# Performance work log

Measured on AMD Instinct MI355X. Metric: run time of the kernel, lower is better.

The kernel has to match this reference:

```python
import jax, jax.numpy as jnp
import numpy as np

B, HQ, HK, S, D, HID, BS = 2, 32, 8, 8192, 128, 128, 16
NB = S // BS  # 512 pooled blocks


def rotate_half(x):
    h = x.shape[-1] // 2
    return jnp.concatenate([-x[..., h:], x[..., :h]], axis=-1)


def pool_cat(x):
    # avg + max pooling over block_size along the sequence dim, concat on feature dim
    b, h, s, d = x.shape
    xb = x.reshape(b, h, s // BS, BS, d)
    return jnp.concatenate([xb.mean(axis=3), xb.max(axis=3)], axis=-1)  # [b,h,NB,2d]


def setup_inputs() -> dict:
    key = jax.random.key(0)
    k0, k1, k2, k3 = jax.random.split(key, 4)
    q = jax.random.normal(k0, (B, HQ, S, D), jnp.float32)
    k = jax.random.normal(k1, (B, HK, S, D), jnp.float32)
    wq = jax.random.normal(k2, (HQ, 2 * D, HID), jnp.float32) / np.float32(np.sqrt(2 * D))
    wk = jax.random.normal(k3, (HK, 2 * D, HID), jnp.float32) / np.float32(np.sqrt(2 * D))
    # causal block mask
    mask = jnp.broadcast_to(jnp.tril(jnp.ones((NB, NB), bool))[None, None], (B, 1, NB, NB))
    # RoPE tables over pooled positions
    pos = jnp.arange(NB, dtype=jnp.float32)
    inv_freq = 1.0 / (10000.0 ** (jnp.arange(0, HID, 2, dtype=jnp.float32) / HID))
    freqs = pos[:, None] * inv_freq[None, :]              # [NB, HID/2]
    emb = jnp.concatenate([freqs, freqs], axis=-1)        # [NB, HID]
    cos = jnp.broadcast_to(jnp.cos(emb)[None], (B, NB, HID))
    sin = jnp.broadcast_to(jnp.sin(emb)[None], (B, NB, HID))
    return {"q": q, "k": k, "attention_mask": mask, "cos": cos, "sin": sin, "wq": wq, "wk": wk}


def reference(q, k, attention_mask, cos, sin, wq, wk):
    # pooled multi-head linear projections
    qh = jnp.einsum('bhnc,hcd->bhnd', pool_cat(q), wq)   # [B,HQ,NB,HID]
    kh = jnp.einsum('bhnc,hcd->bhnd', pool_cat(k), wk)   # [B,HK,NB,HID]
    # RoPE (unsqueeze_dim=1)
    c, s = cos[:, None], sin[:, None]
    qh = qh * c + rotate_half(qh) * s
    kh = kh * c + rotate_half(kh) * s
    # GQA: repeat kv heads
    kh = jnp.repeat(kh, HQ // HK, axis=1)                # [B,HQ,NB,HID]
    attn = jnp.einsum('bhqd,bhkd->bhqk', qh, kh) / jnp.sqrt(jnp.float32(HID))
    attn = jnp.where(attention_mask, attn, jnp.float32(-1e9))
    return jax.nn.softmax(attn, axis=-1)
```

## Files before the change

### kernel.cpp

```cpp
#include <hip/hip_runtime.h>

namespace {
constexpr int BB  = 2;
constexpr int HQ  = 32;
constexpr int HK  = 8;
constexpr int S   = 8192;
constexpr int D   = 128;
constexpr int HID = 128;
constexpr int BS  = 16;
constexpr int NB  = 512;
constexpr int C2D = 256;
constexpr int WTR = 512;
constexpr int BLK = 4096;
}

typedef __attribute__((ext_vector_type(8))) short short8;
typedef __attribute__((ext_vector_type(4))) float f32x4;

__device__ inline unsigned short f2bf(float f) {
  unsigned u = __builtin_bit_cast(unsigned, f);
  unsigned r = u + 0x7fff + ((u >> 16) & 1);
  return (unsigned short)(r >> 16);
}
__device__ inline float bf2f(unsigned short s) {
  unsigned u = ((unsigned)s) << 16;
  return __builtin_bit_cast(float, u);
}

__global__ __launch_bounds__(256) void wprep_kernel(
    const float* __restrict__ wq, const float* __restrict__ wk,
    unsigned short* __restrict__ wT)
{
  __shared__ float ts[32 * 33];
  const int t  = threadIdx.x;
  const int kc = blockIdx.x;
  const int hy = blockIdx.y;
  const float* w = (hy < HQ) ? (wq + (size_t)hy * C2D * HID)
                             : (wk + (size_t)(hy - HQ) * C2D * HID);
  for (int nc = 0; nc < 4; ++nc) {
    __syncthreads();
    {
      const int r = t >> 3, c4 = t & 7;
      *(float4*)&ts[r * 33 + 4 * c4] =
          *(const float4*)(w + (size_t)(kc * 32 + r) * HID + nc * 32 + 4 * c4);
    }
    __syncthreads();
    {
      const int n = t >> 3, g = t & 7;
      const int cb = 8 * (g & 3);
      short8 v;
#pragma unroll
      for (int j = 0; j < 8; ++j) {
        const float f = ts[(cb + j) * 33 + n];
        const unsigned short h = f2bf(f);
        v[j] = (short)((g < 4) ? h : f2bf(f - bf2f(h)));
      }
      unsigned short* dst = wT + ((size_t)hy * HID + nc * 32 + n) * WTR +
                            ((g < 4) ? 0 : 256) + kc * 32 + cb;
      *(short8*)dst = v;
    }
  }
}

__global__ __launch_bounds__(256) void pool_gemm_rope_kernel(
    const float* __restrict__ qx, const float* __restrict__ kx,
    const unsigned short* __restrict__ wT,
    const float* __restrict__ cosp, const float* __restrict__ sinp,
    unsigned short* __restrict__ qhb, unsigned short* __restrict__ khb)
{
  constexpr int AST = 520;
  constexpr int CST = 132;
  __shared__ unsigned short As[32 * AST];
  float* Cs = (float*)As;

  const int t  = threadIdx.x;
  const int n0 = blockIdx.x * 32;
  const int hy = blockIdx.y;
  const int b  = blockIdx.z;

  const float* x; unsigned short* o; int H; int h; bool isq;
  if (hy < HQ) { x = qx; o = qhb; H = HQ; h = hy; isq = true; }
  else         { x = kx; o = khb; H = HK; h = hy - HQ; isq = false; }

  const float* xb = x + (((size_t)b * H + h) * S + (size_t)n0 * BS) * D;
  for (int it = t; it < 32 * 32; it += 256) {
    const int m = it >> 5, d4 = it & 31;
    const f32x4* p = (const f32x4*)(xb + (size_t)m * BS * D) + d4;
    f32x4 v = __builtin_nontemporal_load(p);
    float sx = v.x, sy = v.y, sz = v.z, sw = v.w;
    float mx = v.x, my = v.y, mz = v.z, mw = v.w;
#pragma unroll
    for (int i = 1; i < BS; ++i) {
      v = __builtin_nontemporal_load(p + i * (D / 4));
      sx += v.x; sy += v.y; sz += v.z; sw += v.w;
      mx = fmaxf(mx, v.x); my = fmaxf(my, v.y);
      mz = fmaxf(mz, v.z); mw = fmaxf(mw, v.w);
    }
    const float inv16 = 1.0f / 16.0f;
    float mn[4] = {sx * inv16, sy * inv16, sz * inv16, sw * inv16};
    float mv[4] = {mx, my, mz, mw};
    ushort4 mh, ml, xh, xl;
    mh.x = f2bf(mn[0]); ml.x = f2bf(mn[0] - bf2f(mh.x));
    mh.y = f2bf(mn[1]); ml.y = f2bf(mn[1] - bf2f(mh.y));
    mh.z = f2bf(mn[2]); ml.z = f2bf(mn[2] - bf2f(mh.z));
    mh.w = f2bf(mn[3]); ml.w = f2bf(mn[3] - bf2f(mh.w));
    xh.x = f2bf(mv[0]); xl.x = f2bf(mv[0] - bf2f(xh.x));
    xh.y = f2bf(mv[1]); xl.y = f2bf(mv[1] - bf2f(xh.y));
    xh.z = f2bf(mv[2]); xl.z = f2bf(mv[2] - bf2f(xh.z));
    xh.w = f2bf(mv[3]); xl.w = f2bf(mv[3] - bf2f(xh.w));
    unsigned short* row = &As[m * AST];
    *(ushort4*)(row + 4 * d4)       = mh;
    *(ushort4*)(row + 256 + 4 * d4) = ml;
    *(ushort4*)(row + 128 + 4 * d4) = xh;
    *(ushort4*)(row + 384 + 4 * d4) = xl;
  }
  __syncthreads();

  const int w    = t >> 6;
  const int lane = t & 63;
  const int col  = lane & 15;
  const int quad = lane >> 4;
  const int mtile = w & 1;
  const int nbase = (w >> 1) * 64;

  const unsigned short* arow = &As[(size_t)(mtile * 16 + col) * AST + quad * 8];
  const unsigned short* bp = wT + ((size_t)hy * HID + nbase + col) * WTR + quad * 8;

  f32x4 acc[4];
#pragma unroll
  for (int i = 0; i < 4; ++i) acc[i] = (f32x4){0.f, 0.f, 0.f, 0.f};

#pragma unroll
  for (int ks = 0; ks < 8; ++ks) {
    const short8 ahi = *(const short8*)(arow + ks * 32);
    const short8 alo = *(const short8*)(arow + 256 + ks * 32);
#pragma unroll
    for (int nt = 0; nt < 4; ++nt) {
      const short8 bhi = *(const short8*)(bp + (size_t)nt * 16 * WTR + ks * 32);
      const short8 blo = *(const short8*)(bp + (size_t)nt * 16 * WTR + 256 + ks * 32);
      acc[nt] = __builtin_amdgcn_mfma_f32_16x16x32_bf16(ahi, bhi, acc[nt], 0, 0, 0);
      acc[nt] = __builtin_amdgcn_mfma_f32_16x16x32_bf16(ahi, blo, acc[nt], 0, 0, 0);
      acc[nt] = __builtin_amdgcn_mfma_f32_16x16x32_bf16(alo, bhi, acc[nt], 0, 0, 0);
    }
  }
  __syncthreads();

#pragma unroll
  for (int nt = 0; nt < 4; ++nt)
#pragma unroll
    for (int r = 0; r < 4; ++r)
      Cs[(size_t)(mtile * 16 + quad * 4 + r) * CST + nbase + nt * 16 + col] =
          acc[nt][r];
  __syncthreads();

  const int dt = t & 31, mt = t >> 5;
  const int d0 = dt * 4, m0 = mt * 4;
  const float sgn = (d0 < 64) ? -1.0f : 1.0f;
  const float qscale = isq ? 0.08838834764831843f : 1.0f;
  float4 ov[4];
#pragma unroll
  for (int i = 0; i < 4; ++i) {
    const int n = n0 + m0 + i;
    const float4 cv = *(const float4*)(cosp + ((size_t)b * NB + n) * HID + d0);
    const float4 sv = *(const float4*)(sinp + ((size_t)b * NB + n) * HID + d0);
    const float4 cur = *(const float4*)&Cs[(m0 + i) * CST + d0];
    const float4 pr  = *(const float4*)&Cs[(m0 + i) * CST + (d0 ^ 64)];
    ov[i].x = (cur.x * cv.x + sgn * pr.x * sv.x) * qscale;
    ov[i].y = (cur.y * cv.y + sgn * pr.y * sv.y) * qscale;
    ov[i].z = (cur.z * cv.z + sgn * pr.z * sv.z) * qscale;
    ov[i].w = (cur.w * cv.w + sgn * pr.w * sv.w) * qscale;
  }
  __syncthreads();
#pragma unroll
  for (int i = 0; i < 4; ++i)
    *(float4*)&Cs[(m0 + i) * CST + d0] = ov[i];
  __syncthreads();

  unsigned short* obase = o + ((size_t)b * H + h) * (size_t)(32 * BLK) +
                          (size_t)(n0 >> 4) * BLK;
#pragma unroll
  for (int j = 0; j < 4; ++j) {
    const int c = t + 256 * j;
    const int k16c = c >> 9;
    const int fi   = (c >> 6) & 7;
    const int ln   = c & 63;
    const int colr = ln & 15, quadr = ln >> 4;
    const int n = k16c * 16 + colr;
    const int dstart = (fi & 3) * 32 + quadr * 8;
    const float* src = &Cs[n * CST + dstart];
    short8 outv;
    if (fi < 4) {
#pragma unroll
      for (int e = 0; e < 8; ++e) outv[e] = (short)f2bf(src[e]);
    } else {
#pragma unroll
      for (int e = 0; e < 8; ++e) {
        const float f = src[e];
        outv[e] = (short)f2bf(f - bf2f(f2bf(f)));
      }
    }
    *(short8*)(obase + (size_t)k16c * BLK + (fi * 64 + ln) * 8) = outv;
  }
}

__global__ __launch_bounds__(256) void attn_kernel(
    const unsigned short* __restrict__ qhb,
    const unsigned short* __restrict__ khb,
    float* __restrict__ out)
{
  constexpr int PST = 516;
  __shared__ float Ps[16 * PST];
  __shared__ float rs_lds[16];

  const int t = threadIdx.x;
  const int w = t >> 6;
  const int lane = t & 63;
  const int col = lane & 15;
  const int quad = lane >> 4;
  const int strip = blockIdx.x;
  const int h = blockIdx.y;
  const int b = blockIdx.z;

  const unsigned short* qfb = qhb + (((size_t)b * HQ + h) * 32 + strip) * BLK;
  const unsigned short* kfb = khb + (((size_t)b * HK + (h >> 2)) * 32) * BLK;
  float* obase = out + (((size_t)b * HQ + h) * NB + (size_t)strip * 16) * NB;

  if (t < 16) rs_lds[t] = 0.f;
  {
    const f32x4 z = {0.f, 0.f, 0.f, 0.f};
#pragma unroll
    for (int j = 0; j < 8; ++j) {
      const int c = t + 256 * j;
      const int row = c >> 7, c4 = c & 127;
      *(f32x4*)&Ps[row * PST + 4 * c4] = z;
    }
  }
  __syncthreads();

  short8 qf[8];
#pragma unroll
  for (int fi = 0; fi < 8; ++fi)
    qf[fi] = *(const short8*)(qfb + (fi * 64 + lane) * 8);

  const int n = (w <= strip) ? ((strip - w) >> 2) + 1 : 0;

  float rs[4] = {0.f, 0.f, 0.f, 0.f};

#pragma unroll
  for (int ti = 0; ti < 8; ++ti) {
    if (ti < n) {
      const int k16 = w + 4 * ti;
      const unsigned short* kp = kfb + (size_t)k16 * BLK + lane * 8;
      short8 kf[8];
#pragma unroll
      for (int fi = 0; fi < 8; ++fi)
        kf[fi] = *(const short8*)(kp + fi * 512);
      f32x4 accA = {0.f, 0.f, 0.f, 0.f};
      f32x4 accB = {0.f, 0.f, 0.f, 0.f};
      f32x4 accC = {0.f, 0.f, 0.f, 0.f};
#pragma unroll
      for (int f = 0; f < 4; ++f) {
        accA = __builtin_amdgcn_mfma_f32_16x16x32_bf16(qf[f],     kf[f],     accA, 0, 0, 0);
        accB = __builtin_amdgcn_mfma_f32_16x16x32_bf16(qf[f],     kf[4 + f], accB, 0, 0, 0);
        accC = __builtin_amdgcn_mfma_f32_16x16x32_bf16(qf[4 + f], kf[f],     accC, 0, 0, 0);
      }
      const bool diag = (k16 == strip);
#pragma unroll
      for (int r = 0; r < 4; ++r) {
        float v = __expf(accA[r] + accB[r] + accC[r]);
        if (diag && col > quad * 4 + r) v = 0.f;
        Ps[(quad * 4 + r) * PST + k16 * 16 + col] = v;
        rs[r] += v;
      }
    }
  }

#pragma unroll
  for (int r = 0; r < 4; ++r) {
    float v = rs[r];
    v += __shfl_xor(v, 1, 64);
    v += __shfl_xor(v, 2, 64);
    v += __shfl_xor(v, 4, 64);
    v += __shfl_xor(v, 8, 64);
    if (col == 0) atomicAdd(&rs_lds[quad * 4 + r], v);
  }
  __syncthreads();

  if (t < 16) rs_lds[t] = 1.0f / rs_lds[t];
  __syncthreads();

#pragma unroll
  for (int j = 0; j < 8; ++j) {
    const int c = t + 256 * j;
    const int row = c >> 7, c4 = c & 127;
    f32x4 v = *(const f32x4*)&Ps[row * PST + 4 * c4];
    v *= rs_lds[row];
    __builtin_nontemporal_store(v, (f32x4*)(obase + (size_t)row * NB + 4 * c4));
  }
}

extern "C" void kernel_launch(void* const* d_in, const int* in_sizes, int n_in,
                              void* d_out, int out_size, void* d_ws, size_t ws_size,
                              hipStream_t stream)
{
  const float* q    = (const float*)d_in[0];
  const float* k    = (const float*)d_in[1];
  const float* cosp = (const float*)d_in[3];
  const float* sinp = (const float*)d_in[4];
  const float* wq   = (const float*)d_in[5];
  const float* wk   = (const float*)d_in[6];
  float* out = (float*)d_out;

  unsigned short* qhb = (unsigned short*)d_ws;
  unsigned short* khb = qhb + (size_t)BB * HQ * 32 * BLK;
  unsigned short* wTp = khb + (size_t)BB * HK * 32 * BLK;

  hipLaunchKernelGGL(wprep_kernel, dim3(8, HQ + HK), dim3(256),
                     0, stream, wq, wk, wTp);
  hipLaunchKernelGGL(pool_gemm_rope_kernel, dim3(NB / 32, HQ + HK, BB), dim3(256),
                     0, stream, q, k, wTp, cosp, sinp, qhb, khb);
  hipLaunchKernelGGL(attn_kernel, dim3(32, HQ, BB), dim3(256),
                     0, stream, qhb, khb, out);
}
```

Measured before the change: 452.0 us.

## Remap workgroups across XCDs, fuse RoPE into bf16 store, hoist Q loads

Both kernels now remap the flat block index so that consecutive logical workgroups land on the same XCD (index mod 8), which should improve L2 locality for the shared K heads and weights. In the projection kernel the separate RoPE pass, with its LDS round-trip and two barriers, is folded into the bf16 hi/lo split store loop. The attention kernel issues its Q-fragment global loads before zeroing LDS and the barrier, so load latency overlaps that setup. The remap relies on hardcoded grid sizes (16x40x2 and 32x32x2).

```diff
diff --git a/kernel.cpp b/kernel.cpp
--- a/kernel.cpp
+++ b/kernel.cpp
@@ -74,9 +74,11 @@
   float* Cs = (float*)As;
 
   const int t  = threadIdx.x;
-  const int n0 = blockIdx.x * 32;
-  const int hy = blockIdx.y;
-  const int b  = blockIdx.z;
+  const int flat = blockIdx.x + 16 * (blockIdx.y + 40 * blockIdx.z);
+  const int wg   = (flat & 7) * 160 + (flat >> 3);
+  const int n0 = (wg & 15) * 32;
+  const int hy = (wg >> 4) % 40;
+  const int b  = wg / 640;
 
   const float* x; unsigned short* o; int H; int h; bool isq;
   if (hy < HQ) { x = qx; o = qhb; H = HQ; h = hy; isq = true; }
@@ -153,29 +155,7 @@
           acc[nt][r];
   __syncthreads();
 
-  const int dt = t & 31, mt = t >> 5;
-  const int d0 = dt * 4, m0 = mt * 4;
-  const float sgn = (d0 < 64) ? -1.0f : 1.0f;
   const float qscale = isq ? 0.08838834764831843f : 1.0f;
-  float4 ov[4];
-#pragma unroll
-  for (int i = 0; i < 4; ++i) {
-    const int n = n0 + m0 + i;
-    const float4 cv = *(const float4*)(cosp + ((size_t)b * NB + n) * HID + d0);
-    const float4 sv = *(const float4*)(sinp + ((size_t)b * NB + n) * HID + d0);
-    const float4 cur = *(const float4*)&Cs[(m0 + i) * CST + d0];
-    const float4 pr  = *(const float4*)&Cs[(m0 + i) * CST + (d0 ^ 64)];
-    ov[i].x = (cur.x * cv.x + sgn * pr.x * sv.x) * qscale;
-    ov[i].y = (cur.y * cv.y + sgn * pr.y * sv.y) * qscale;
-    ov[i].z = (cur.z * cv.z + sgn * pr.z * sv.z) * qscale;
-    ov[i].w = (cur.w * cv.w + sgn * pr.w * sv.w) * qscale;
-  }
-  __syncthreads();
-#pragma unroll
-  for (int i = 0; i < 4; ++i)
-    *(float4*)&Cs[(m0 + i) * CST + d0] = ov[i];
-  __syncthreads();
-
   unsigned short* obase = o + ((size_t)b * H + h) * (size_t)(32 * BLK) +
                           (size_t)(n0 >> 4) * BLK;
 #pragma unroll
@@ -185,19 +165,38 @@
     const int fi   = (c >> 6) & 7;
     const int ln   = c & 63;
     const int colr = ln & 15, quadr = ln >> 4;
-    const int n = k16c * 16 + colr;
+    const int nrow = k16c * 16 + colr;
     const int dstart = (fi & 3) * 32 + quadr * 8;
-    const float* src = &Cs[n * CST + dstart];
+    const float sgn = (dstart < 64) ? -1.0f : 1.0f;
+    const float* curp = &Cs[nrow * CST + dstart];
+    const float* prp  = &Cs[nrow * CST + (dstart ^ 64)];
+    const float* cvp = cosp + ((size_t)b * NB + n0 + nrow) * HID + dstart;
+    const float* svp = sinp + ((size_t)b * NB + n0 + nrow) * HID + dstart;
+    const float4 cu0 = *(const float4*)(curp);
+    const float4 cu1 = *(const float4*)(curp + 4);
+    const float4 pr0 = *(const float4*)(prp);
+    const float4 pr1 = *(const float4*)(prp + 4);
+    const float4 cv0 = *(const float4*)(cvp);
+    const float4 cv1 = *(const float4*)(cvp + 4);
+    const float4 sv0 = *(const float4*)(svp);
+    const float4 sv1 = *(const float4*)(svp + 4);
+    float rv[8];
+    rv[0] = (cu0.x * cv0.x + sgn * pr0.x * sv0.x) * qscale;
+    rv[1] = (cu0.y * cv0.y + sgn * pr0.y * sv0.y) * qscale;
+    rv[2] = (cu0.z * cv0.z + sgn * pr0.z * sv0.z) * qscale;
+    rv[3] = (cu0.w * cv0.w + sgn * pr0.w * sv0.w) * qscale;
+    rv[4] = (cu1.x * cv1.x + sgn * pr1.x * sv1.x) * qscale;
+    rv[5] = (cu1.y * cv1.y + sgn * pr1.y * sv1.y) * qscale;
+    rv[6] = (cu1.z * cv1.z + sgn * pr1.z * sv1.z) * qscale;
+    rv[7] = (cu1.w * cv1.w + sgn * pr1.w * sv1.w) * qscale;
     short8 outv;
     if (fi < 4) {
 #pragma unroll
-      for (int e = 0; e < 8; ++e) outv[e] = (short)f2bf(src[e]);
+      for (int e = 0; e < 8; ++e) outv[e] = (short)f2bf(rv[e]);
     } else {
 #pragma unroll
-      for (int e = 0; e < 8; ++e) {
-        const float f = src[e];
-        outv[e] = (short)f2bf(f - bf2f(f2bf(f)));
-      }
+      for (int e = 0; e < 8; ++e)
+        outv[e] = (short)f2bf(rv[e] - bf2f(f2bf(rv[e])));
     }
     *(short8*)(obase + (size_t)k16c * BLK + (fi * 64 + ln) * 8) = outv;
   }
@@ -217,13 +216,20 @@
   const int lane = t & 63;
   const int col = lane & 15;
   const int quad = lane >> 4;
-  const int strip = blockIdx.x;
-  const int h = blockIdx.y;
-  const int b = blockIdx.z;
+  const int flat = blockIdx.x + 32 * (blockIdx.y + 32 * blockIdx.z);
+  const int wg   = (flat & 7) * 256 + (flat >> 3);
+  const int strip = wg & 31;
+  const int h = (wg >> 5) & 31;
+  const int b = wg >> 10;
 
   const unsigned short* qfb = qhb + (((size_t)b * HQ + h) * 32 + strip) * BLK;
   const unsigned short* kfb = khb + (((size_t)b * HK + (h >> 2)) * 32) * BLK;
   float* obase = out + (((size_t)b * HQ + h) * NB + (size_t)strip * 16) * NB;
+
+  short8 qf[8];
+#pragma unroll
+  for (int fi = 0; fi < 8; ++fi)
+    qf[fi] = *(const short8*)(qfb + (fi * 64 + lane) * 8);
 
   if (t < 16) rs_lds[t] = 0.f;
   {
@@ -236,11 +242,6 @@
     }
   }
   __syncthreads();
-
-  short8 qf[8];
-#pragma unroll
-  for (int fi = 0; fi < 8; ++fi)
-    qf[fi] = *(const short8*)(qfb + (fi * 64 + lane) * 8);
 
   const int n = (w <= strip) ? ((strip - w) >> 2) + 1 : 0;
 
```

New measurement: 449.2 us. Within noise of the previous version (-0.6%).
